# Performance work log

Hardware: AMD Instinct MI355X
Metric: run time of the kernel (lower is better)

Reference implementation:

```python
import jax, jax.numpy as jnp
import numpy as np
import math

B, L, D, H = 4, 2048, 1024, 16
HD = D // H  # head dim = 64


def setup_inputs() -> dict:
    key = jax.random.key(0)
    ks = jax.random.split(key, 5)
    s = 1.0 / math.sqrt(D)
    return {
        "x": jax.random.normal(ks[0], (B, L, D), dtype=jnp.float32),
        "Wqkv": jax.random.normal(ks[1], (D, 3 * D), dtype=jnp.float32) * s,
        "bqkv": jax.random.normal(ks[2], (3 * D,), dtype=jnp.float32) * 0.02,
        "Wproj": jax.random.normal(ks[3], (D, D), dtype=jnp.float32) * s,
        "bproj": jax.random.normal(ks[4], (D,), dtype=jnp.float32) * 0.02,
    }


def reference(x, Wqkv, bqkv, Wproj, bproj):
    Bsz, Ls, Ds = x.shape
    qkv = x @ Wqkv + bqkv                     # [B, L, 3D]
    q, k, v = jnp.split(qkv, 3, axis=-1)      # each [B, L, D]

    def heads(t):  # [B, L, D] -> [B, H, L, HD]
        return t.reshape(Bsz, Ls, H, HD).transpose(0, 2, 1, 3)

    q, k, v = heads(q), heads(k), heads(v)
    att = jnp.einsum("bhqd,bhkd->bhqk", q, k) / jnp.sqrt(jnp.float32(HD))
    causal = jnp.tril(jnp.ones((Ls, Ls), dtype=bool))
    att = jnp.where(causal[None, None], att, -jnp.inf)
    att = jax.nn.softmax(att, axis=-1)
    y = jnp.einsum("bhqk,bhkd->bhqd", att, v)  # [B, H, L, HD]
    y = y.transpose(0, 2, 1, 3).reshape(Bsz, Ls, Ds)
    return y @ Wproj + bproj
```

## Files before the change

### kernel.cpp

```cpp
#include <hip/hip_runtime.h>


typedef __bf16 bf16x2 __attribute__((ext_vector_type(2)));
typedef __bf16 bf16x8 __attribute__((ext_vector_type(8)));
typedef float f32x4 __attribute__((ext_vector_type(4)));
typedef float f32x16 __attribute__((ext_vector_type(16)));
typedef unsigned u32x4 __attribute__((ext_vector_type(4)));

#define MFMA16(a, b, c) __builtin_amdgcn_mfma_f32_16x16x32_bf16(a, b, c, 0, 0, 0)
#define MFMA32(a, b, c) __builtin_amdgcn_mfma_f32_32x32x16_bf16(a, b, c, 0, 0, 0)

__device__ __forceinline__ void gload_lds16(const __bf16* g, __bf16* l) {
    __builtin_amdgcn_global_load_lds(
        (const __attribute__((address_space(1))) void*)g,
        (__attribute__((address_space(3))) void*)l, 16, 0, 0);
}

__device__ __forceinline__ unsigned pkbf(float a, float b) {
    bf16x2 t = {(__bf16)a, (__bf16)b};
    return __builtin_bit_cast(unsigned, t);
}

__global__ void convert_kernel(const float* __restrict__ in, __bf16* __restrict__ out)
{
    int i = (blockIdx.x * 256 + threadIdx.x) * 8;
    f32x4 lo = *(const f32x4*)&in[i];
    f32x4 hi = *(const f32x4*)&in[i + 4];
    bf16x8 o;
#pragma unroll
    for (int j = 0; j < 4; ++j) { o[j] = (__bf16)lo[j]; o[j + 4] = (__bf16)hi[j]; }
    *(bf16x8*)&out[i] = o;
}

__global__ void transpose_convert_kernel(const float* __restrict__ in,
                                         __bf16* __restrict__ out, int R, int C)
{
    __shared__ __bf16 t[32][33];
    const int c0 = blockIdx.x * 32, r0 = blockIdx.y * 32;
    const int tx = threadIdx.x & 31, ty = threadIdx.x >> 5;
#pragma unroll
    for (int j = 0; j < 4; ++j) {
        int r = ty + j * 8;
        t[tx][r] = (__bf16)in[(size_t)(r0 + r) * C + c0 + tx];
    }
    __syncthreads();
#pragma unroll
    for (int j = 0; j < 4; ++j) {
        int r = ty + j * 8;
        out[(size_t)(c0 + r) * R + r0 + tx] = t[r][tx];
    }
}

#define GEMM_TILE_LOOP(Abase, Bbase)                                               \
    for (int k0 = 0; k0 < 1024; k0 += 32) {                                        \
        __syncthreads();                                                           \
        _Pragma("unroll")                                                          \
        for (int i = 0; i < 2; ++i) {                                              \
            int wl = w * 2 + i;                                                    \
            int r = wl * 16 + (lane >> 2);                                         \
            int c = ((lane & 3) ^ ((r >> 1) & 3)) * 8;                             \
            gload_lds16(&Abase[(size_t)(m0 + r) * 1024 + k0 + c], &As[wl * 512]);  \
            gload_lds16(&Bbase[(size_t)(n0 + r) * 1024 + k0 + c], &Bs[wl * 512]);  \
        }                                                                          \
        __syncthreads();                                                           \
        bf16x8 af[4], bfr[4];                                                      \
        _Pragma("unroll")                                                          \
        for (int mf = 0; mf < 4; ++mf) {                                           \
            int rr = wr * 64 + mf * 16 + row;                                      \
            af[mf] = *(const bf16x8*)&As[rr * 32 + ((g ^ ((rr >> 1) & 3)) * 8)];   \
        }                                                                          \
        _Pragma("unroll")                                                          \
        for (int nf = 0; nf < 4; ++nf) {                                           \
            int rr = wc * 64 + nf * 16 + row;                                      \
            bfr[nf] = *(const bf16x8*)&Bs[rr * 32 + ((g ^ ((rr >> 1) & 3)) * 8)];  \
        }                                                                          \
        _Pragma("unroll")                                                          \
        for (int mf = 0; mf < 4; ++mf)                                             \
            _Pragma("unroll")                                                      \
            for (int nf = 0; nf < 4; ++nf)                                         \
                acc[mf][nf] = MFMA16(af[mf], bfr[nf], acc[mf][nf]);                \
    }

__global__ __launch_bounds__(256, 2)
void qkv_gemm_kernel(const __bf16* __restrict__ A, const __bf16* __restrict__ Bt,
                     const float* __restrict__ bias,
                     __bf16* __restrict__ q2, __bf16* __restrict__ k2,
                     __bf16* __restrict__ v2)
{
    __shared__ __bf16 stage[16384];
    __bf16* const As = stage;
    __bf16* const Bs = stage + 4096;
    const int tid = threadIdx.x;
    const int lane = tid & 63;
    const int w = tid >> 6;
    const int wr = w >> 1, wc = w & 1;
    const int row = lane & 15, g = lane >> 4;
    const int m0 = blockIdx.x * 128;
    const int n0 = blockIdx.y * 128;

    const f32x4 fzero = {0.f, 0.f, 0.f, 0.f};
    f32x4 acc[4][4];
#pragma unroll
    for (int a = 0; a < 4; ++a)
#pragma unroll
        for (int b = 0; b < 4; ++b) acc[a][b] = fzero;

    GEMM_TILE_LOOP(A, Bt)

    __syncthreads();
    const int part = n0 >> 10;
    const float QSCL = 0.18033688f;
#pragma unroll
    for (int mf = 0; mf < 4; ++mf)
#pragma unroll
        for (int nf = 0; nf < 4; ++nf) {
            int nl = nf * 16 + row;
            float bv = bias[n0 + wc * 64 + nl];
#pragma unroll
            for (int i = 0; i < 4; ++i) {
                int ml = mf * 16 + g * 4 + i;
                float fv = acc[mf][nf][i] + bv;
                if (part == 0) fv *= QSCL;
                int c, off;
                if (part == 2) {
                    c = (ml >> 5) * 4 + (nl >> 5) * 2 + ((ml >> 4) & 1);
                    off = ((ml >> 2) & 1) * 256 + (nl & 31) * 8 +
                          ((ml & 3) | (((ml >> 3) & 1) << 2));
                } else {
                    c = (ml >> 5) * 4 + (nl >> 4);
                    off = ((nl >> 3) & 1) * 256 + (ml & 31) * 8 + (nl & 7);
                }
                stage[w * 4096 + c * 512 + off] = (__bf16)fv;
            }
        }
    {
        const int b = m0 >> 11;
        const int lbase5 = (m0 & 2047) >> 5;
        const int hh = ((n0 & 1023) >> 6) + wc;
        const size_t bh64 = (size_t)(b * 16 + hh) * 64;
        __bf16* dst = part == 0 ? q2 : (part == 1 ? k2 : v2);
#pragma unroll
        for (int c = 0; c < 8; ++c) {
            bf16x8 val = *(const bf16x8*)&stage[w * 4096 + c * 512 + lane * 8];
            size_t gbase = ((bh64 + lbase5 + wr * 2 + (c >> 2)) * 4 + (c & 3)) * 512;
            *(bf16x8*)&dst[gbase + lane * 8] = val;
        }
    }
}

__global__ __launch_bounds__(256, 2)
void proj_gemm_kernel(const __bf16* __restrict__ A, const __bf16* __restrict__ Bt,
                      const float* __restrict__ bias, float* __restrict__ out)
{
    __shared__ __bf16 As[128 * 32];
    __shared__ __bf16 Bs[128 * 32];
    const int tid = threadIdx.x;
    const int lane = tid & 63;
    const int w = tid >> 6;
    const int wr = w >> 1, wc = w & 1;
    const int row = lane & 15, g = lane >> 4;
    const int m0 = blockIdx.x * 128;
    const int n0 = blockIdx.y * 128;

    const f32x4 fzero = {0.f, 0.f, 0.f, 0.f};
    f32x4 acc[4][4];
#pragma unroll
    for (int a = 0; a < 4; ++a)
#pragma unroll
        for (int b = 0; b < 4; ++b) acc[a][b] = fzero;

    GEMM_TILE_LOOP(A, Bt)

#pragma unroll
    for (int mf = 0; mf < 4; ++mf)
#pragma unroll
        for (int nf = 0; nf < 4; ++nf) {
            int n = n0 + wc * 64 + nf * 16 + row;
            float bv = bias[n];
#pragma unroll
            for (int i = 0; i < 4; ++i) {
                int mm = m0 + wr * 64 + mf * 16 + g * 4 + i;
                out[(size_t)mm * 1024 + n] = acc[mf][nf][i] + bv;
            }
        }
}

__global__ __launch_bounds__(128, 2)
void attn_kernel(const __bf16* __restrict__ Q2, const __bf16* __restrict__ K2,
                 const __bf16* __restrict__ V2, __bf16* __restrict__ Yw)
{
    const int tid = threadIdx.x;
    const int lane = tid & 63;
    const int wv = tid >> 6;
    const int col = lane & 31;
    const int hi = lane >> 5;
    const int i0 = blockIdx.x;
    const int bh = (i0 & 7) * 8 + ((i0 >> 3) & 7);
    const int t = (i0 >> 6) * 2 + wv;
    const int tB = 63 - t;
    const int qA = t * 32;
    const int qB = tB * 32;
    const size_t tb = (size_t)bh * 64;

    bf16x8 qfA[4], qfB[4];
#pragma unroll
    for (int dc = 0; dc < 4; ++dc) {
        qfA[dc] = *(const bf16x8*)&Q2[((tb + t) * 4 + dc) * 512 + lane * 8];
        qfB[dc] = *(const bf16x8*)&Q2[((tb + tB) * 4 + dc) * 512 + lane * 8];
    }

    bf16x8 ones;
#pragma unroll
    for (int j = 0; j < 8; ++j) ones[j] = (__bf16)1.0f;

    f32x16 CZ;
#pragma unroll
    for (int i = 0; i < 16; ++i) CZ[i] = 0.f;

    f32x16 OtA[2], OtB[2], OsA, OsB;
#pragma unroll
    for (int dt = 0; dt < 2; ++dt)
#pragma unroll
        for (int i = 0; i < 16; ++i) { OtA[dt][i] = 0.f; OtB[dt][i] = 0.f; }
#pragma unroll
    for (int i = 0; i < 16; ++i) { OsA[i] = 0.f; OsB[i] = 0.f; }

    auto smxpack = [&](f32x16& st, f32x16& Os, bool diag,
                       bf16x8& pa0, bf16x8& pa1) {
        if (diag) {
#pragma unroll
            for (int r = 0; r < 16; ++r) {
                int crow = (r & 3) + 8 * (r >> 2) + 4 * hi;
                if (crow > col) st[r] = -1e30f;
            }
        }
#pragma unroll
        for (int r = 0; r < 16; ++r) st[r] = exp2f(st[r]);
        u32x4 w0 = {pkbf(st[0], st[1]), pkbf(st[2], st[3]),
                    pkbf(st[4], st[5]), pkbf(st[6], st[7])};
        u32x4 w1 = {pkbf(st[8], st[9]), pkbf(st[10], st[11]),
                    pkbf(st[12], st[13]), pkbf(st[14], st[15])};
        pa0 = __builtin_bit_cast(bf16x8, w0);
        pa1 = __builtin_bit_cast(bf16x8, w1);
        Os = MFMA32(ones, pa0, Os);
        Os = MFMA32(ones, pa1, Os);
    };

    const __bf16* kp = K2 + tb * 2048 + lane * 8;
    const __bf16* vp = V2 + tb * 2048 + lane * 8;

    bf16x8 kfP[4], vfP[4];
#pragma unroll
    for (int dc = 0; dc < 4; ++dc) {
        kfP[dc] = *(const bf16x8*)&kp[dc * 512];
        vfP[dc] = *(const bf16x8*)&vp[dc * 512];
    }

    const int nsteps = tB + 1;
    for (int kt = 0; kt < nsteps; ++kt) {
        const bool dual = (kt <= t);
        const __bf16* kpn = kp + 2048;
        const __bf16* vpn = vp + 2048;
        bf16x8 kfQ[4], vfQ[4];
#pragma unroll
        for (int dc = 0; dc < 4; ++dc) {
            kfQ[dc] = *(const bf16x8*)&kpn[dc * 512];
            vfQ[dc] = *(const bf16x8*)&vpn[dc * 512];
        }

        f32x16 stA, stB;
        __builtin_amdgcn_s_setprio(1);
        stB = MFMA32(kfP[0], qfB[0], CZ);
        stB = MFMA32(kfP[1], qfB[1], stB);
        stB = MFMA32(kfP[2], qfB[2], stB);
        stB = MFMA32(kfP[3], qfB[3], stB);
        if (dual) {
            stA = MFMA32(kfP[0], qfA[0], CZ);
            stA = MFMA32(kfP[1], qfA[1], stA);
            stA = MFMA32(kfP[2], qfA[2], stA);
            stA = MFMA32(kfP[3], qfA[3], stA);
        }
        __builtin_amdgcn_s_setprio(0);

        bf16x8 paA0, paA1, paB0, paB1;
        smxpack(stB, OsB, kt == tB, paB0, paB1);
        if (dual) smxpack(stA, OsA, kt == t, paA0, paA1);

        __builtin_amdgcn_s_setprio(1);
        OtB[0] = MFMA32(vfP[0], paB0, OtB[0]);
        OtB[0] = MFMA32(vfP[1], paB1, OtB[0]);
        OtB[1] = MFMA32(vfP[2], paB0, OtB[1]);
        OtB[1] = MFMA32(vfP[3], paB1, OtB[1]);
        if (dual) {
            OtA[0] = MFMA32(vfP[0], paA0, OtA[0]);
            OtA[0] = MFMA32(vfP[1], paA1, OtA[0]);
            OtA[1] = MFMA32(vfP[2], paA0, OtA[1]);
            OtA[1] = MFMA32(vfP[3], paA1, OtA[1]);
        }
        __builtin_amdgcn_s_setprio(0);

#pragma unroll
        for (int dc = 0; dc < 4; ++dc) { kfP[dc] = kfQ[dc]; vfP[dc] = vfQ[dc]; }
        kp = kpn; vp = vpn;
    }

    const int b = bh >> 4, h = bh & 15;
    const float invA = 1.f / OsA[0], invB = 1.f / OsB[0];
    __bf16* yrowA = Yw + ((size_t)(b * 2048 + qA + col)) * 1024 + h * 64;
    __bf16* yrowB = Yw + ((size_t)(b * 2048 + qB + col)) * 1024 + h * 64;
#pragma unroll
    for (int dt = 0; dt < 2; ++dt)
#pragma unroll
        for (int rg = 0; rg < 4; ++rg) {
            int d0 = dt * 32 + rg * 8 + hi * 4;
            unsigned lo = pkbf(OtA[dt][rg * 4 + 0] * invA, OtA[dt][rg * 4 + 1] * invA);
            unsigned h2 = pkbf(OtA[dt][rg * 4 + 2] * invA, OtA[dt][rg * 4 + 3] * invA);
            *(unsigned long long*)&yrowA[d0] =
                (unsigned long long)lo | ((unsigned long long)h2 << 32);
            lo = pkbf(OtB[dt][rg * 4 + 0] * invB, OtB[dt][rg * 4 + 1] * invB);
            h2 = pkbf(OtB[dt][rg * 4 + 2] * invB, OtB[dt][rg * 4 + 3] * invB);
            *(unsigned long long*)&yrowB[d0] =
                (unsigned long long)lo | ((unsigned long long)h2 << 32);
        }
}

extern "C" void kernel_launch(void* const* d_in, const int* in_sizes, int n_in,
                              void* d_out, int out_size, void* d_ws, size_t ws_size,
                              hipStream_t stream)
{
    const float* x     = (const float*)d_in[0];
    const float* wqkv  = (const float*)d_in[1];
    const float* bqkv  = (const float*)d_in[2];
    const float* wproj = (const float*)d_in[3];
    const float* bproj = (const float*)d_in[4];
    float* out = (float*)d_out;

    const size_t E = (size_t)4 * 16 * 2048 * 64;
    __bf16* q2     = (__bf16*)d_ws;
    __bf16* k2     = q2 + E;
    __bf16* v2     = k2 + E;
    __bf16* xb     = v2 + E;
    __bf16* y      = xb;
    __bf16* wqkvT  = xb + E;
    __bf16* wprojT = wqkvT + (size_t)3072 * 1024;

    convert_kernel<<<4096, 256, 0, stream>>>(x, xb);
    transpose_convert_kernel<<<dim3(96, 32), 256, 0, stream>>>(wqkv, wqkvT, 1024, 3072);
    transpose_convert_kernel<<<dim3(32, 32), 256, 0, stream>>>(wproj, wprojT, 1024, 1024);
    qkv_gemm_kernel<<<dim3(64, 24), 256, 0, stream>>>(xb, wqkvT, bqkv, q2, k2, v2);
    attn_kernel<<<1024, 128, 0, stream>>>(q2, k2, v2, y);
    proj_gemm_kernel<<<dim3(64, 8), 256, 0, stream>>>(y, wprojT, bproj, out);
}
```

Before: 167.3 us.

## Fuse conversion kernels, double GEMM K-tile to 64, vectorize V epilogue stores

The three fp32-to-bf16 conversion and transpose launches are merged into a single kernel that dispatches on block index, removing two launch overheads. Both GEMMs now use a 64-wide K step with an 8-way XOR swizzle, which halves the number of barrier and load phases per tile and doubles LDS tile size. The V-part epilogue writes four packed bf16 values per store instead of scalar stores. The larger LDS footprint may reduce occupancy in the projection GEMM.

After: 152.7 us. 8.7% less time.

```diff
diff --git a/kernel.cpp b/kernel.cpp
--- a/kernel.cpp
+++ b/kernel.cpp
@@ -2,6 +2,7 @@
 
 
 typedef __bf16 bf16x2 __attribute__((ext_vector_type(2)));
+typedef __bf16 bf16x4 __attribute__((ext_vector_type(4)));
 typedef __bf16 bf16x8 __attribute__((ext_vector_type(8)));
 typedef float f32x4 __attribute__((ext_vector_type(4)));
 typedef float f32x16 __attribute__((ext_vector_type(16)));
@@ -21,22 +22,33 @@
     return __builtin_bit_cast(unsigned, t);
 }
 
-__global__ void convert_kernel(const float* __restrict__ in, __bf16* __restrict__ out)
-{
-    int i = (blockIdx.x * 256 + threadIdx.x) * 8;
-    f32x4 lo = *(const f32x4*)&in[i];
-    f32x4 hi = *(const f32x4*)&in[i + 4];
-    bf16x8 o;
-#pragma unroll
-    for (int j = 0; j < 4; ++j) { o[j] = (__bf16)lo[j]; o[j + 4] = (__bf16)hi[j]; }
-    *(bf16x8*)&out[i] = o;
-}
-
-__global__ void transpose_convert_kernel(const float* __restrict__ in,
-                                         __bf16* __restrict__ out, int R, int C)
-{
+__global__ void fused_convert_kernel(const float* __restrict__ x, __bf16* __restrict__ xb,
+                                     const float* __restrict__ wqkv, __bf16* __restrict__ wqkvT,
+                                     const float* __restrict__ wproj, __bf16* __restrict__ wprojT)
+{
+    const int blk = blockIdx.x;
+    if (blk < 4096) {
+        int i = (blk * 256 + threadIdx.x) * 8;
+        f32x4 lo = *(const f32x4*)&x[i];
+        f32x4 hi = *(const f32x4*)&x[i + 4];
+        bf16x8 o;
+#pragma unroll
+        for (int j = 0; j < 4; ++j) { o[j] = (__bf16)lo[j]; o[j + 4] = (__bf16)hi[j]; }
+        *(bf16x8*)&xb[i] = o;
+        return;
+    }
     __shared__ __bf16 t[32][33];
-    const int c0 = blockIdx.x * 32, r0 = blockIdx.y * 32;
+    const float* in;
+    __bf16* out;
+    int R, C, bx, by;
+    if (blk < 7168) {
+        int b2 = blk - 4096;
+        bx = b2 % 96; by = b2 / 96; in = wqkv; out = wqkvT; R = 1024; C = 3072;
+    } else {
+        int b2 = blk - 7168;
+        bx = b2 % 32; by = b2 / 32; in = wproj; out = wprojT; R = 1024; C = 1024;
+    }
+    const int c0 = bx * 32, r0 = by * 32;
     const int tx = threadIdx.x & 31, ty = threadIdx.x >> 5;
 #pragma unroll
     for (int j = 0; j < 4; ++j) {
@@ -52,33 +64,40 @@
 }
 
 #define GEMM_TILE_LOOP(Abase, Bbase)                                               \
-    for (int k0 = 0; k0 < 1024; k0 += 32) {                                        \
+    for (int k0 = 0; k0 < 1024; k0 += 64) {                                        \
         __syncthreads();                                                           \
         _Pragma("unroll")                                                          \
-        for (int i = 0; i < 2; ++i) {                                              \
-            int wl = w * 2 + i;                                                    \
-            int r = wl * 16 + (lane >> 2);                                         \
-            int c = ((lane & 3) ^ ((r >> 1) & 3)) * 8;                             \
-            gload_lds16(&Abase[(size_t)(m0 + r) * 1024 + k0 + c], &As[wl * 512]);  \
-            gload_lds16(&Bbase[(size_t)(n0 + r) * 1024 + k0 + c], &Bs[wl * 512]);  \
+        for (int l = 0; l < 4; ++l) {                                              \
+            int base = l * 256 + w * 64;                                           \
+            int r = (base >> 3) + (lane >> 3);                                     \
+            int c = (lane & 7) ^ (r & 7);                                          \
+            gload_lds16(&Abase[(size_t)(m0 + r) * 1024 + k0 + c * 8], &As[base * 8]); \
+            gload_lds16(&Bbase[(size_t)(n0 + r) * 1024 + k0 + c * 8], &Bs[base * 8]); \
         }                                                                          \
         __syncthreads();                                                           \
-        bf16x8 af[4], bfr[4];                                                      \
+        bf16x8 af[2][4], bfr[2][4];                                                \
         _Pragma("unroll")                                                          \
-        for (int mf = 0; mf < 4; ++mf) {                                           \
-            int rr = wr * 64 + mf * 16 + row;                                      \
-            af[mf] = *(const bf16x8*)&As[rr * 32 + ((g ^ ((rr >> 1) & 3)) * 8)];   \
+        for (int kk = 0; kk < 2; ++kk) {                                           \
+            _Pragma("unroll")                                                      \
+            for (int mf = 0; mf < 4; ++mf) {                                       \
+                int rr = wr * 64 + mf * 16 + row;                                  \
+                af[kk][mf] = *(const bf16x8*)                                      \
+                    &As[rr * 64 + (((kk * 4 + g) ^ (rr & 7)) * 8)];                \
+            }                                                                      \
+            _Pragma("unroll")                                                      \
+            for (int nf = 0; nf < 4; ++nf) {                                       \
+                int rr = wc * 64 + nf * 16 + row;                                  \
+                bfr[kk][nf] = *(const bf16x8*)                                     \
+                    &Bs[rr * 64 + (((kk * 4 + g) ^ (rr & 7)) * 8)];                \
+            }                                                                      \
         }                                                                          \
         _Pragma("unroll")                                                          \
-        for (int nf = 0; nf < 4; ++nf) {                                           \
-            int rr = wc * 64 + nf * 16 + row;                                      \
-            bfr[nf] = *(const bf16x8*)&Bs[rr * 32 + ((g ^ ((rr >> 1) & 3)) * 8)];  \
-        }                                                                          \
-        _Pragma("unroll")                                                          \
-        for (int mf = 0; mf < 4; ++mf)                                             \
+        for (int kk = 0; kk < 2; ++kk)                                             \
             _Pragma("unroll")                                                      \
-            for (int nf = 0; nf < 4; ++nf)                                         \
-                acc[mf][nf] = MFMA16(af[mf], bfr[nf], acc[mf][nf]);                \
+            for (int mf = 0; mf < 4; ++mf)                                         \
+                _Pragma("unroll")                                                  \
+                for (int nf = 0; nf < 4; ++nf)                                     \
+                    acc[mf][nf] = MFMA16(af[kk][mf], bfr[kk][nf], acc[mf][nf]);    \
     }
 
 __global__ __launch_bounds__(256, 2)
@@ -89,7 +108,7 @@
 {
     __shared__ __bf16 stage[16384];
     __bf16* const As = stage;
-    __bf16* const Bs = stage + 4096;
+    __bf16* const Bs = stage + 8192;
     const int tid = threadIdx.x;
     const int lane = tid & 63;
     const int w = tid >> 6;
@@ -110,29 +129,40 @@
     __syncthreads();
     const int part = n0 >> 10;
     const float QSCL = 0.18033688f;
-#pragma unroll
-    for (int mf = 0; mf < 4; ++mf)
-#pragma unroll
-        for (int nf = 0; nf < 4; ++nf) {
-            int nl = nf * 16 + row;
-            float bv = bias[n0 + wc * 64 + nl];
-#pragma unroll
-            for (int i = 0; i < 4; ++i) {
-                int ml = mf * 16 + g * 4 + i;
-                float fv = acc[mf][nf][i] + bv;
-                if (part == 0) fv *= QSCL;
-                int c, off;
-                if (part == 2) {
-                    c = (ml >> 5) * 4 + (nl >> 5) * 2 + ((ml >> 4) & 1);
-                    off = ((ml >> 2) & 1) * 256 + (nl & 31) * 8 +
-                          ((ml & 3) | (((ml >> 3) & 1) << 2));
-                } else {
-                    c = (ml >> 5) * 4 + (nl >> 4);
-                    off = ((nl >> 3) & 1) * 256 + (ml & 31) * 8 + (nl & 7);
+    if (part == 2) {
+#pragma unroll
+        for (int mf = 0; mf < 4; ++mf)
+#pragma unroll
+            for (int nf = 0; nf < 4; ++nf) {
+                int nl = nf * 16 + row;
+                float bv = bias[n0 + wc * 64 + nl];
+                bf16x4 pv;
+#pragma unroll
+                for (int i = 0; i < 4; ++i)
+                    pv[i] = (__bf16)(acc[mf][nf][i] + bv);
+                int c = (mf >> 1) * 4 + (nl >> 5) * 2 + (mf & 1);
+                int off0 = (g & 1) * 256 + (nl & 31) * 8 + ((g >> 1) & 1) * 4;
+                *(unsigned long long*)&stage[w * 4096 + c * 512 + off0] =
+                    __builtin_bit_cast(unsigned long long, pv);
+            }
+    } else {
+#pragma unroll
+        for (int mf = 0; mf < 4; ++mf)
+#pragma unroll
+            for (int nf = 0; nf < 4; ++nf) {
+                int nl = nf * 16 + row;
+                float bv = bias[n0 + wc * 64 + nl];
+#pragma unroll
+                for (int i = 0; i < 4; ++i) {
+                    int ml = mf * 16 + g * 4 + i;
+                    float fv = acc[mf][nf][i] + bv;
+                    if (part == 0) fv *= QSCL;
+                    int c = (ml >> 5) * 4 + (nl >> 4);
+                    int off = ((nl >> 3) & 1) * 256 + (ml & 31) * 8 + (nl & 7);
+                    stage[w * 4096 + c * 512 + off] = (__bf16)fv;
                 }
-                stage[w * 4096 + c * 512 + off] = (__bf16)fv;
             }
-        }
+    }
     {
         const int b = m0 >> 11;
         const int lbase5 = (m0 & 2047) >> 5;
@@ -152,8 +182,8 @@
 void proj_gemm_kernel(const __bf16* __restrict__ A, const __bf16* __restrict__ Bt,
                       const float* __restrict__ bias, float* __restrict__ out)
 {
-    __shared__ __bf16 As[128 * 32];
-    __shared__ __bf16 Bs[128 * 32];
+    __shared__ __bf16 As[128 * 64];
+    __shared__ __bf16 Bs[128 * 64];
     const int tid = threadIdx.x;
     const int lane = tid & 63;
     const int w = tid >> 6;
@@ -344,9 +374,7 @@
     __bf16* wqkvT  = xb + E;
     __bf16* wprojT = wqkvT + (size_t)3072 * 1024;
 
-    convert_kernel<<<4096, 256, 0, stream>>>(x, xb);
-    transpose_convert_kernel<<<dim3(96, 32), 256, 0, stream>>>(wqkv, wqkvT, 1024, 3072);
-    transpose_convert_kernel<<<dim3(32, 32), 256, 0, stream>>>(wproj, wprojT, 1024, 1024);
+    fused_convert_kernel<<<8192, 256, 0, stream>>>(x, xb, wqkv, wqkvT, wproj, wprojT);
     qkv_gemm_kernel<<<dim3(64, 24), 256, 0, stream>>>(xb, wqkvT, bqkv, q2, k2, v2);
     attn_kernel<<<1024, 128, 0, stream>>>(q2, k2, v2, y);
     proj_gemm_kernel<<<dim3(64, 8), 256, 0, stream>>>(y, wprojT, bproj, out);
```
